# Kernel optimization log

Hardware: AMD Instinct MI355X
Metric: run time of the kernel (lower is better)

Reference implementation:

```python
import jax, jax.numpy as jnp
import numpy as np

B, L, E, H = 2, 2048, 1024, 16
HD = E // H  # 64
THETA = 10000.0


def setup_inputs() -> dict:
    key = jax.random.key(0)
    ks = jax.random.split(key, 9)
    s = 1.0 / np.sqrt(E)
    return {
        "x": jax.random.normal(ks[0], (B, L, E), jnp.float32),
        "Wq": jax.random.normal(ks[1], (E, E), jnp.float32) * s,
        "bq": jax.random.normal(ks[2], (E,), jnp.float32) * 0.01,
        "Wk": jax.random.normal(ks[3], (E, E), jnp.float32) * s,
        "bk": jax.random.normal(ks[4], (E,), jnp.float32) * 0.01,
        "Wv": jax.random.normal(ks[5], (E, E), jnp.float32) * s,
        "bv": jax.random.normal(ks[6], (E,), jnp.float32) * 0.01,
        "Wo": jax.random.normal(ks[7], (E, E), jnp.float32) * s,
        "bo": jax.random.normal(ks[8], (E,), jnp.float32) * 0.01,
    }


def _rope_tables(seq_len, dim, dtype):
    # lucidrains RotaryEmbedding: inv_freq over even indices, each freq repeated twice (interleaved)
    inv_freq = 1.0 / (THETA ** (jnp.arange(0, dim, 2, dtype=jnp.float32) / dim))
    freqs = jnp.arange(seq_len, dtype=jnp.float32)[:, None] * inv_freq[None, :]  # [L, dim/2]
    freqs = jnp.repeat(freqs, 2, axis=-1)  # [L, dim] -> f0,f0,f1,f1,...
    return jnp.cos(freqs).astype(dtype), jnp.sin(freqs).astype(dtype)


def _rotate_half(x):
    # interleaved pairs (x0, x1) -> (-x1, x0)
    x2 = x.reshape(*x.shape[:-1], -1, 2)
    x2 = jnp.stack([-x2[..., 1], x2[..., 0]], axis=-1)
    return x2.reshape(x.shape)


def _apply_rope(x, cos, sin):
    # x: [B, H, L, HD]; cos/sin: [L, HD]
    return x * cos[None, None] + _rotate_half(x) * sin[None, None]


def reference(x, Wq, bq, Wk, bk, Wv, bv, Wo, bo):
    b, l, e = x.shape
    q = (x @ Wq.T + bq).reshape(b, l, H, HD).transpose(0, 2, 1, 3)
    k = (x @ Wk.T + bk).reshape(b, l, H, HD).transpose(0, 2, 1, 3)
    v = (x @ Wv.T + bv).reshape(b, l, H, HD).transpose(0, 2, 1, 3)

    cos, sin = _rope_tables(l, HD, x.dtype)
    q = _apply_rope(q, cos, sin)
    k = _apply_rope(k, cos, sin)

    scale = 1.0 / np.sqrt(HD)
    scores = jnp.einsum("bhsd,bhed->bhse", q, k) * scale  # [B,H,L,L]
    attn = jax.nn.softmax(scores, axis=-1)
    out = jnp.einsum("bhse,bhed->bhsd", attn, v)  # [B,H,L,HD]
    out = out.transpose(0, 2, 1, 3).reshape(b, l, e)
    return out @ Wo.T + bo
```

## Files before the change

kernel.cpp:

```cpp
#include <hip/hip_runtime.h>

typedef unsigned short u16;
typedef __bf16 bf16x8 __attribute__((ext_vector_type(8)));
typedef float f32x4 __attribute__((ext_vector_type(4)));

#define LOG2E 1.4426950408889634f
#define EXP2(x) __builtin_amdgcn_exp2f(x)
#define NFM (-11.0f * LOG2E)

__device__ __forceinline__ u16 f2bf(float f) {
  unsigned int u = __float_as_uint(f);
  u += 0x7fffu + ((u >> 16) & 1u);
  return (u16)(u >> 16);
}

__device__ __forceinline__ void gld16(u16* lds, const u16* g) {
  __builtin_amdgcn_global_load_lds((const __attribute__((address_space(1))) unsigned int*)g,
                                   (__attribute__((address_space(3))) unsigned int*)lds,
                                   16, 0, 0);
}

__device__ __forceinline__ bf16x8 ldsv(const u16* p) {
  return *(const bf16x8*)p;
}

union U8 { uint4 u; bf16x8 v; };

__global__ __launch_bounds__(256) void k_prep(const float* __restrict__ x,
    const float* __restrict__ wq, const float* __restrict__ wk,
    const float* __restrict__ wv, const float* __restrict__ wo,
    u16* __restrict__ xb, u16* __restrict__ wqkvb, u16* __restrict__ wob) {
  unsigned gid = blockIdx.x * 256u + threadIdx.x;
  const float4* src;
  u16* dst;
  unsigned off;
  if (gid < 1048576u)      { src = (const float4*)x;  dst = xb;              off = gid; }
  else if (gid < 1310720u) { src = (const float4*)wq; dst = wqkvb;           off = gid - 1048576u; }
  else if (gid < 1572864u) { src = (const float4*)wk; dst = wqkvb + 1048576; off = gid - 1310720u; }
  else if (gid < 1835008u) { src = (const float4*)wv; dst = wqkvb + 2097152; off = gid - 1572864u; }
  else                     { src = (const float4*)wo; dst = wob;             off = gid - 1835008u; }
  float4 f = src[off];
  ushort4 o;
  o.x = f2bf(f.x); o.y = f2bf(f.y); o.z = f2bf(f.z); o.w = f2bf(f.w);
  ((ushort4*)dst)[off] = o;
}

__global__ __launch_bounds__(256) void k_rope(float* __restrict__ cosT, float* __restrict__ sinT) {
  int t = blockIdx.x * 256 + threadIdx.x;
  int l = t >> 5, i = t & 31;
  float inv = powf(10000.0f, -(float)i * (1.0f / 32.0f));
  float ang = (float)l * inv;
  float s, c;
  sincosf(ang, &s, &c);
  cosT[t] = c;
  sinT[t] = s;
}

__device__ __forceinline__ void gemm_loop(const u16* __restrict__ A, const u16* __restrict__ B,
                                          int m0, int n0, u16* As, u16* Bs, f32x4 acc[4][4]) {
  const int tid = threadIdx.x;
  const int lane = tid & 63, wave = tid >> 6;
  const int quad = lane >> 4, l16 = lane & 15;
  const int wm = wave & 1, wn = wave >> 1;

#pragma unroll
  for (int i = 0; i < 4; ++i)
#pragma unroll
    for (int j = 0; j < 4; ++j)
      acc[i][j] = (f32x4){0.f, 0.f, 0.f, 0.f};

  for (int kt = 0; kt < 16; ++kt) {
    int kb = kt * 64;
#pragma unroll
    for (int it = 0; it < 4; ++it) {
      int idx = it * 256 + tid;
      int row = idx >> 3, c8 = idx & 7;
      gld16(As + idx * 8, A + (long)(m0 + row) * 1024 + kb + c8 * 8);
      gld16(Bs + idx * 8, B + (long)(n0 + row) * 1024 + kb + c8 * 8);
    }
    __syncthreads();
#pragma unroll
    for (int kk = 0; kk < 2; ++kk) {
      bf16x8 a[4], b[4];
#pragma unroll
      for (int i = 0; i < 4; ++i)
        a[i] = ldsv(As + (wm * 64 + i * 16 + l16) * 64 + kk * 32 + quad * 8);
#pragma unroll
      for (int j = 0; j < 4; ++j)
        b[j] = ldsv(Bs + (wn * 64 + j * 16 + l16) * 64 + kk * 32 + quad * 8);
#pragma unroll
      for (int i = 0; i < 4; ++i)
#pragma unroll
        for (int j = 0; j < 4; ++j)
          acc[i][j] = __builtin_amdgcn_mfma_f32_16x16x32_bf16(a[i], b[j], acc[i][j], 0, 0, 0);
    }
    __syncthreads();
  }
}

__global__ __launch_bounds__(256) void k_qkv(const u16* __restrict__ xb, const u16* __restrict__ wqkvb,
    const float* __restrict__ bq, const float* __restrict__ bk, const float* __restrict__ bv,
    const float* __restrict__ cosT, const float* __restrict__ sinT,
    u16* __restrict__ Qg, u16* __restrict__ Kg, u16* __restrict__ VTg) {
  __shared__ __align__(16) u16 S[128 * 132];
  u16* As = S;
  u16* Bs = S + 8192;
  f32x4 acc[4][4];
  int m0 = blockIdx.y * 128, n0 = blockIdx.x * 128;
  gemm_loop(xb, wqkvb, m0, n0, As, Bs, acc);

  const int tid = threadIdx.x, lane = tid & 63, wave = tid >> 6;
  const int quad = lane >> 4, l16 = lane & 15;
  const int wm = wave & 1, wn = wave >> 1;
  const int qsel = n0 >> 10;
  const int b = m0 >> 11;
  const int mb0 = m0 & 2047;

  if (qsel < 2) {
    const float* bp = qsel ? bk : bq;
#pragma unroll
    for (int j = 0; j < 4; ++j) {
      int nl = wn * 64 + j * 16 + l16;
      int n = n0 + nl;
      int fcol = n & 1023;
      int d = fcol & 63;
      int pi = d >> 1;
      float bias = bp[fcol];
      float sgn = (d & 1) ? 1.0f : -1.0f;
#pragma unroll
      for (int i = 0; i < 4; ++i) {
#pragma unroll
        for (int r = 0; r < 4; ++r) {
          int ml = wm * 64 + i * 16 + quad * 4 + r;
          int l = mb0 + ml;
          float v = acc[i][j][r] + bias;
          float partner = __shfl_xor(v, 1);
          float c = cosT[l * 32 + pi], s = sinT[l * 32 + pi];
          float o = fmaf(v, c, sgn * partner * s);
          if (qsel == 0) o *= 0.125f;
          S[ml * 132 + nl] = f2bf(o);
        }
      }
    }
    __syncthreads();
    u16* dstb = (qsel == 0) ? Qg : Kg;
#pragma unroll
    for (int t = 0; t < 16; ++t) {
      int idx = t * 256 + tid;
      int ml = idx >> 5, c4 = idx & 31;
      int n = n0 + c4 * 4;
      int h = (n & 1023) >> 6;
      int d = n & 63;
      *(uint2*)(dstb + (((long)b * 16 + h) * 2048 + mb0 + ml) * 64 + d) =
          *(const uint2*)(S + ml * 132 + c4 * 4);
    }
  } else {
#pragma unroll
    for (int j = 0; j < 4; ++j) {
      int nl = wn * 64 + j * 16 + l16;
      float bias = bv[(n0 + nl) & 1023];
#pragma unroll
      for (int i = 0; i < 4; ++i) {
        int mb = wm * 64 + i * 16 + quad * 4;
        unsigned u0 = (unsigned)f2bf(acc[i][j][0] + bias) | ((unsigned)f2bf(acc[i][j][1] + bias) << 16);
        unsigned u1 = (unsigned)f2bf(acc[i][j][2] + bias) | ((unsigned)f2bf(acc[i][j][3] + bias) << 16);
        *(uint2*)(S + nl * 132 + mb) = make_uint2(u0, u1);
      }
    }
    __syncthreads();
#pragma unroll
    for (int t = 0; t < 16; ++t) {
      int idx = t * 256 + tid;
      int nl = idx >> 5, c4 = idx & 31;
      int vcol = (n0 & 1023) + nl;
      int h = vcol >> 6, d = vcol & 63;
      *(uint2*)(VTg + (((long)b * 16 + h) * 64 + d) * 2048 + mb0 + c4 * 4) =
          *(const uint2*)(S + nl * 132 + c4 * 4);
    }
  }
}

__global__ __launch_bounds__(256, 2) void k_attn(const u16* __restrict__ Qg, const u16* __restrict__ Kg,
    const u16* __restrict__ VTg, u16* __restrict__ Ctx) {
  __shared__ __align__(16) char smem[34816];
  u16* Ks = (u16*)smem;
  u16* Vs = (u16*)(smem + 16384);
  const int tid = threadIdx.x, lane = tid & 63, wave = tid >> 6;
  const int quad = lane >> 4, l16 = lane & 15;
  const int wm = wave & 1, wsn = wave >> 1;
  const int bh = blockIdx.y;
  const int m0 = blockIdx.x * 128;
  const u16* Qb = Qg + (long)bh * 2048 * 64;
  const u16* Kb = Kg + (long)bh * 2048 * 64;
  const u16* Vb = VTg + (long)bh * 64 * 2048;

  bf16x8 qf[4][2];
#pragma unroll
  for (int mt = 0; mt < 4; ++mt)
#pragma unroll
    for (int kk = 0; kk < 2; ++kk)
      qf[mt][kk] = *(const bf16x8*)(Qb + (long)(m0 + wm * 64 + mt * 16 + l16) * 64 + kk * 32 + quad * 8);

  f32x4 oacc[4][4];
  float rs[4];
#pragma unroll
  for (int dt = 0; dt < 4; ++dt)
#pragma unroll
    for (int mt = 0; mt < 4; ++mt)
      oacc[dt][mt] = (f32x4){0.f, 0.f, 0.f, 0.f};
#pragma unroll
  for (int mt = 0; mt < 4; ++mt) rs[mt] = 0.f;

  for (int st = 0; st < 16; ++st) {
    int s0 = st * 128;
#pragma unroll
    for (int it = 0; it < 4; ++it) {
      int idx = it * 256 + tid;
      int row = idx >> 3, c8 = idx & 7;
      gld16(Ks + idx * 8, Kb + (long)(s0 + row) * 64 + c8 * 8);
    }
#pragma unroll
    for (int it = 0; it < 4; ++it) {
      int idx = it * 256 + tid;
      int row = idx >> 4, g = idx & 15;
      uint4 vv = *(const uint4*)(Vb + (long)row * 2048 + s0 + g * 8);
      u16* wp = Vs + row * 132 + g * 8;
      *(uint2*)wp = make_uint2(vv.x, vv.y);
      *(uint2*)(wp + 4) = make_uint2(vv.z, vv.w);
    }
    __syncthreads();

    f32x4 sacc[4][4];
#pragma unroll
    for (int ct = 0; ct < 4; ++ct)
#pragma unroll
      for (int mt = 0; mt < 4; ++mt)
        sacc[ct][mt] = (f32x4){0.f, 0.f, 0.f, 0.f};
#pragma unroll
    for (int kk = 0; kk < 2; ++kk) {
      bf16x8 kf[4];
#pragma unroll
      for (int ct = 0; ct < 4; ++ct)
        kf[ct] = ldsv(Ks + (wsn * 64 + ct * 16 + l16) * 64 + kk * 32 + quad * 8);
#pragma unroll
      for (int ct = 0; ct < 4; ++ct)
#pragma unroll
        for (int mt = 0; mt < 4; ++mt)
          sacc[ct][mt] = __builtin_amdgcn_mfma_f32_16x16x32_bf16(kf[ct], qf[mt][kk], sacc[ct][mt], 0, 0, 0);
    }

#pragma unroll
    for (int c = 0; c < 2; ++c) {
      unsigned pk[2][4][2];
#pragma unroll
      for (int t = 0; t < 2; ++t) {
        int ct = c * 2 + t;
#pragma unroll
        for (int mt = 0; mt < 4; ++mt) {
          unsigned b[4];
          float sum = 0.f;
#pragma unroll
          for (int r = 0; r < 4; ++r) {
            float e = EXP2(fmaf(sacc[ct][mt][r], LOG2E, NFM));
            b[r] = __float_as_uint(e);
            sum += __uint_as_float(b[r] & 0xffff0000u);
          }
          rs[mt] += sum;
          pk[t][mt][0] = __builtin_amdgcn_perm(b[1], b[0], 0x07060302u);
          pk[t][mt][1] = __builtin_amdgcn_perm(b[3], b[2], 0x07060302u);
        }
      }
#pragma unroll
      for (int dt = 0; dt < 4; ++dt) {
        const u16* vp = Vs + (dt * 16 + l16) * 132 + wsn * 64 + c * 32 + quad * 4;
        uint2 lo = *(const uint2*)vp;
        uint2 hi = *(const uint2*)(vp + 16);
        U8 vfu; vfu.u = make_uint4(lo.x, lo.y, hi.x, hi.y);
#pragma unroll
        for (int mt = 0; mt < 4; ++mt) {
          U8 pfu; pfu.u = make_uint4(pk[0][mt][0], pk[0][mt][1], pk[1][mt][0], pk[1][mt][1]);
          oacc[dt][mt] = __builtin_amdgcn_mfma_f32_16x16x32_bf16(vfu.v, pfu.v, oacc[dt][mt], 0, 0, 0);
        }
      }
    }
    __syncthreads();
  }

  float* mbuf = (float*)smem;
  if (wsn == 1) {
#pragma unroll
    for (int dt = 0; dt < 4; ++dt)
#pragma unroll
      for (int mt = 0; mt < 4; ++mt)
#pragma unroll
        for (int r = 0; r < 4; ++r)
          mbuf[(wm * 68 + dt * 16 + mt * 4 + r) * 64 + lane] = oacc[dt][mt][r];
#pragma unroll
    for (int mt = 0; mt < 4; ++mt)
      mbuf[(wm * 68 + 64 + mt) * 64 + lane] = rs[mt];
  }
  __syncthreads();
  if (wsn == 0) {
#pragma unroll
    for (int dt = 0; dt < 4; ++dt)
#pragma unroll
      for (int mt = 0; mt < 4; ++mt)
#pragma unroll
        for (int r = 0; r < 4; ++r)
          oacc[dt][mt][r] += mbuf[(wm * 68 + dt * 16 + mt * 4 + r) * 64 + lane];
#pragma unroll
    for (int mt = 0; mt < 4; ++mt) {
      rs[mt] += mbuf[(wm * 68 + 64 + mt) * 64 + lane];
      rs[mt] += __shfl_xor(rs[mt], 16);
      rs[mt] += __shfl_xor(rs[mt], 32);
    }
    const int b = bh >> 4, h = bh & 15;
#pragma unroll
    for (int mt = 0; mt < 4; ++mt) {
      float inv = 1.0f / rs[mt];
      int tok = m0 + wm * 64 + mt * 16 + l16;
      u16* cp = Ctx + ((long)(b * 2048 + tok)) * 1024 + h * 64 + quad * 4;
#pragma unroll
      for (int dt = 0; dt < 4; ++dt) {
        float o0 = oacc[dt][mt][0] * inv, o1 = oacc[dt][mt][1] * inv;
        float o2 = oacc[dt][mt][2] * inv, o3 = oacc[dt][mt][3] * inv;
        unsigned u0 = (unsigned)f2bf(o0) | ((unsigned)f2bf(o1) << 16);
        unsigned u1 = (unsigned)f2bf(o2) | ((unsigned)f2bf(o3) << 16);
        *(uint2*)(cp + dt * 16) = make_uint2(u0, u1);
      }
    }
  }
}

__global__ __launch_bounds__(256) void k_out(const u16* __restrict__ Ctx, const u16* __restrict__ wob,
    const float* __restrict__ bo, float* __restrict__ out) {
  __shared__ __align__(16) u16 As[128 * 64];
  __shared__ __align__(16) u16 Bs[128 * 64];
  f32x4 acc[4][4];
  int m0 = blockIdx.y * 128, n0 = blockIdx.x * 128;
  gemm_loop(Ctx, wob, m0, n0, As, Bs, acc);
  const int tid = threadIdx.x, lane = tid & 63, wave = tid >> 6;
  const int quad = lane >> 4, l16 = lane & 15;
  const int wm = wave & 1, wn = wave >> 1;
#pragma unroll
  for (int i = 0; i < 4; ++i)
#pragma unroll
    for (int j = 0; j < 4; ++j) {
      int n = n0 + wn * 64 + j * 16 + l16;
      float b_ = bo[n];
#pragma unroll
      for (int r = 0; r < 4; ++r) {
        int m = m0 + wm * 64 + i * 16 + quad * 4 + r;
        out[(long)m * 1024 + n] = acc[i][j][r] + b_;
      }
    }
}

extern "C" void kernel_launch(void* const* d_in, const int* in_sizes, int n_in,
                              void* d_out, int out_size, void* d_ws, size_t ws_size,
                              hipStream_t stream) {
  const float* x  = (const float*)d_in[0];
  const float* Wq = (const float*)d_in[1];
  const float* bq = (const float*)d_in[2];
  const float* Wk = (const float*)d_in[3];
  const float* bk = (const float*)d_in[4];
  const float* Wv = (const float*)d_in[5];
  const float* bv = (const float*)d_in[6];
  const float* Wo = (const float*)d_in[7];
  const float* bo = (const float*)d_in[8];
  float* out = (float*)d_out;

  char* ws = (char*)d_ws;
  u16* xb    = (u16*)(ws);
  u16* wqkvb = (u16*)(ws + (8ul << 20));
  u16* wob   = (u16*)(ws + (14ul << 20));
  u16* Qg    = (u16*)(ws + (16ul << 20));
  u16* Kg    = (u16*)(ws + (24ul << 20));
  u16* VTg   = (u16*)(ws + (32ul << 20));
  u16* Ctx   = (u16*)(ws + (40ul << 20));
  float* cosT = (float*)(ws + (48ul << 20));
  float* sinT = (float*)(ws + (48ul << 20) + (256ul << 10));

  k_prep<<<dim3(8192), dim3(256), 0, stream>>>(x, Wq, Wk, Wv, Wo, xb, wqkvb, wob);
  k_rope<<<dim3(256), dim3(256), 0, stream>>>(cosT, sinT);
  k_qkv<<<dim3(24, 32), dim3(256), 0, stream>>>(xb, wqkvb, bq, bk, bv, cosT, sinT, Qg, Kg, VTg);
  k_attn<<<dim3(16, 32), dim3(256), 0, stream>>>(Qg, Kg, VTg, Ctx);
  k_out<<<dim3(8, 32), dim3(256), 0, stream>>>(Ctx, wob, bo, out);
}
```

Measured before the change: 220.3 us.

## Fuse rope table into prep, halve attention/out-proj M tiles, swizzle K LDS

Folds the RoPE cos/sin table generation into the prep conversion kernel, removing one launch. Halves the attention query tile to 64 rows, doubles the grid, and raises launch bounds to 4 blocks per CU for more occupancy. It also XOR-swizzles the K tile in LDS to reduce bank conflicts. The output projection moves to 64-row tiles with an inlined GEMM loop so more blocks fill the GPU. The trade-off is less reuse of each K/V tile per block, so global and LDS traffic per output rises.

```diff
diff --git a/kernel.cpp b/kernel.cpp
--- a/kernel.cpp
+++ b/kernel.cpp
@@ -29,8 +29,20 @@
 __global__ __launch_bounds__(256) void k_prep(const float* __restrict__ x,
     const float* __restrict__ wq, const float* __restrict__ wk,
     const float* __restrict__ wv, const float* __restrict__ wo,
-    u16* __restrict__ xb, u16* __restrict__ wqkvb, u16* __restrict__ wob) {
+    u16* __restrict__ xb, u16* __restrict__ wqkvb, u16* __restrict__ wob,
+    float* __restrict__ cosT, float* __restrict__ sinT) {
   unsigned gid = blockIdx.x * 256u + threadIdx.x;
+  if (gid >= 2097152u) {
+    int t = gid - 2097152u;
+    int l = t >> 5, i = t & 31;
+    float inv = powf(10000.0f, -(float)i * (1.0f / 32.0f));
+    float ang = (float)l * inv;
+    float s, c;
+    sincosf(ang, &s, &c);
+    cosT[t] = c;
+    sinT[t] = s;
+    return;
+  }
   const float4* src;
   u16* dst;
   unsigned off;
@@ -45,17 +57,6 @@
   ((ushort4*)dst)[off] = o;
 }
 
-__global__ __launch_bounds__(256) void k_rope(float* __restrict__ cosT, float* __restrict__ sinT) {
-  int t = blockIdx.x * 256 + threadIdx.x;
-  int l = t >> 5, i = t & 31;
-  float inv = powf(10000.0f, -(float)i * (1.0f / 32.0f));
-  float ang = (float)l * inv;
-  float s, c;
-  sincosf(ang, &s, &c);
-  cosT[t] = c;
-  sinT[t] = s;
-}
-
 __device__ __forceinline__ void gemm_loop(const u16* __restrict__ A, const u16* __restrict__ B,
                                           int m0, int n0, u16* As, u16* Bs, f32x4 acc[4][4]) {
   const int tid = threadIdx.x;
@@ -180,7 +181,7 @@
   }
 }
 
-__global__ __launch_bounds__(256, 2) void k_attn(const u16* __restrict__ Qg, const u16* __restrict__ Kg,
+__global__ __launch_bounds__(256, 4) void k_attn(const u16* __restrict__ Qg, const u16* __restrict__ Kg,
     const u16* __restrict__ VTg, u16* __restrict__ Ctx) {
   __shared__ __align__(16) char smem[34816];
   u16* Ks = (u16*)smem;
@@ -188,28 +189,28 @@
   const int tid = threadIdx.x, lane = tid & 63, wave = tid >> 6;
   const int quad = lane >> 4, l16 = lane & 15;
   const int wm = wave & 1, wsn = wave >> 1;
+  const int sw = l16 & 7;
   const int bh = blockIdx.y;
-  const int m0 = blockIdx.x * 128;
+  const int m0 = blockIdx.x * 64;
   const u16* Qb = Qg + (long)bh * 2048 * 64;
   const u16* Kb = Kg + (long)bh * 2048 * 64;
   const u16* Vb = VTg + (long)bh * 64 * 2048;
 
-  bf16x8 qf[4][2];
-#pragma unroll
-  for (int mt = 0; mt < 4; ++mt)
+  bf16x8 qf[2][2];
+#pragma unroll
+  for (int mt = 0; mt < 2; ++mt)
 #pragma unroll
     for (int kk = 0; kk < 2; ++kk)
-      qf[mt][kk] = *(const bf16x8*)(Qb + (long)(m0 + wm * 64 + mt * 16 + l16) * 64 + kk * 32 + quad * 8);
-
-  f32x4 oacc[4][4];
-  float rs[4];
+      qf[mt][kk] = *(const bf16x8*)(Qb + (long)(m0 + wm * 32 + mt * 16 + l16) * 64 + kk * 32 + quad * 8);
+
+  f32x4 oacc[4][2];
+  float rs[2];
 #pragma unroll
   for (int dt = 0; dt < 4; ++dt)
 #pragma unroll
-    for (int mt = 0; mt < 4; ++mt)
+    for (int mt = 0; mt < 2; ++mt)
       oacc[dt][mt] = (f32x4){0.f, 0.f, 0.f, 0.f};
-#pragma unroll
-  for (int mt = 0; mt < 4; ++mt) rs[mt] = 0.f;
+  rs[0] = rs[1] = 0.f;
 
   for (int st = 0; st < 16; ++st) {
     int s0 = st * 128;
@@ -217,7 +218,8 @@
     for (int it = 0; it < 4; ++it) {
       int idx = it * 256 + tid;
       int row = idx >> 3, c8 = idx & 7;
-      gld16(Ks + idx * 8, Kb + (long)(s0 + row) * 64 + c8 * 8);
+      int sc = c8 ^ (row & 7);
+      gld16(Ks + idx * 8, Kb + (long)(s0 + row) * 64 + sc * 8);
     }
 #pragma unroll
     for (int it = 0; it < 4; ++it) {
@@ -230,33 +232,34 @@
     }
     __syncthreads();
 
-    f32x4 sacc[4][4];
+    f32x4 sacc[4][2];
 #pragma unroll
     for (int ct = 0; ct < 4; ++ct)
 #pragma unroll
-      for (int mt = 0; mt < 4; ++mt)
+      for (int mt = 0; mt < 2; ++mt)
         sacc[ct][mt] = (f32x4){0.f, 0.f, 0.f, 0.f};
 #pragma unroll
     for (int kk = 0; kk < 2; ++kk) {
+      int ch = (kk * 4 + quad) ^ sw;
       bf16x8 kf[4];
 #pragma unroll
       for (int ct = 0; ct < 4; ++ct)
-        kf[ct] = ldsv(Ks + (wsn * 64 + ct * 16 + l16) * 64 + kk * 32 + quad * 8);
+        kf[ct] = ldsv(Ks + (wsn * 64 + ct * 16 + l16) * 64 + ch * 8);
 #pragma unroll
       for (int ct = 0; ct < 4; ++ct)
 #pragma unroll
-        for (int mt = 0; mt < 4; ++mt)
+        for (int mt = 0; mt < 2; ++mt)
           sacc[ct][mt] = __builtin_amdgcn_mfma_f32_16x16x32_bf16(kf[ct], qf[mt][kk], sacc[ct][mt], 0, 0, 0);
     }
 
 #pragma unroll
     for (int c = 0; c < 2; ++c) {
-      unsigned pk[2][4][2];
+      unsigned pk[2][2][2];
 #pragma unroll
       for (int t = 0; t < 2; ++t) {
         int ct = c * 2 + t;
 #pragma unroll
-        for (int mt = 0; mt < 4; ++mt) {
+        for (int mt = 0; mt < 2; ++mt) {
           unsigned b[4];
           float sum = 0.f;
 #pragma unroll
@@ -277,7 +280,7 @@
         uint2 hi = *(const uint2*)(vp + 16);
         U8 vfu; vfu.u = make_uint4(lo.x, lo.y, hi.x, hi.y);
 #pragma unroll
-        for (int mt = 0; mt < 4; ++mt) {
+        for (int mt = 0; mt < 2; ++mt) {
           U8 pfu; pfu.u = make_uint4(pk[0][mt][0], pk[0][mt][1], pk[1][mt][0], pk[1][mt][1]);
           oacc[dt][mt] = __builtin_amdgcn_mfma_f32_16x16x32_bf16(vfu.v, pfu.v, oacc[dt][mt], 0, 0, 0);
         }
@@ -291,34 +294,34 @@
 #pragma unroll
     for (int dt = 0; dt < 4; ++dt)
 #pragma unroll
-      for (int mt = 0; mt < 4; ++mt)
+      for (int mt = 0; mt < 2; ++mt)
 #pragma unroll
         for (int r = 0; r < 4; ++r)
-          mbuf[(wm * 68 + dt * 16 + mt * 4 + r) * 64 + lane] = oacc[dt][mt][r];
-#pragma unroll
-    for (int mt = 0; mt < 4; ++mt)
-      mbuf[(wm * 68 + 64 + mt) * 64 + lane] = rs[mt];
+          mbuf[(wm * 34 + dt * 8 + mt * 4 + r) * 64 + lane] = oacc[dt][mt][r];
+#pragma unroll
+    for (int mt = 0; mt < 2; ++mt)
+      mbuf[(wm * 34 + 32 + mt) * 64 + lane] = rs[mt];
   }
   __syncthreads();
   if (wsn == 0) {
 #pragma unroll
     for (int dt = 0; dt < 4; ++dt)
 #pragma unroll
-      for (int mt = 0; mt < 4; ++mt)
+      for (int mt = 0; mt < 2; ++mt)
 #pragma unroll
         for (int r = 0; r < 4; ++r)
-          oacc[dt][mt][r] += mbuf[(wm * 68 + dt * 16 + mt * 4 + r) * 64 + lane];
-#pragma unroll
-    for (int mt = 0; mt < 4; ++mt) {
-      rs[mt] += mbuf[(wm * 68 + 64 + mt) * 64 + lane];
+          oacc[dt][mt][r] += mbuf[(wm * 34 + dt * 8 + mt * 4 + r) * 64 + lane];
+#pragma unroll
+    for (int mt = 0; mt < 2; ++mt) {
+      rs[mt] += mbuf[(wm * 34 + 32 + mt) * 64 + lane];
       rs[mt] += __shfl_xor(rs[mt], 16);
       rs[mt] += __shfl_xor(rs[mt], 32);
     }
     const int b = bh >> 4, h = bh & 15;
 #pragma unroll
-    for (int mt = 0; mt < 4; ++mt) {
+    for (int mt = 0; mt < 2; ++mt) {
       float inv = 1.0f / rs[mt];
-      int tok = m0 + wm * 64 + mt * 16 + l16;
+      int tok = m0 + wm * 32 + mt * 16 + l16;
       u16* cp = Ctx + ((long)(b * 2048 + tok)) * 1024 + h * 64 + quad * 4;
 #pragma unroll
       for (int dt = 0; dt < 4; ++dt) {
@@ -334,23 +337,63 @@
 
 __global__ __launch_bounds__(256) void k_out(const u16* __restrict__ Ctx, const u16* __restrict__ wob,
     const float* __restrict__ bo, float* __restrict__ out) {
-  __shared__ __align__(16) u16 As[128 * 64];
+  __shared__ __align__(16) u16 As[64 * 64];
   __shared__ __align__(16) u16 Bs[128 * 64];
-  f32x4 acc[4][4];
-  int m0 = blockIdx.y * 128, n0 = blockIdx.x * 128;
-  gemm_loop(Ctx, wob, m0, n0, As, Bs, acc);
-  const int tid = threadIdx.x, lane = tid & 63, wave = tid >> 6;
+  const int tid = threadIdx.x;
+  const int lane = tid & 63, wave = tid >> 6;
   const int quad = lane >> 4, l16 = lane & 15;
   const int wm = wave & 1, wn = wave >> 1;
-#pragma unroll
-  for (int i = 0; i < 4; ++i)
+  int m0 = blockIdx.y * 64, n0 = blockIdx.x * 128;
+
+  f32x4 acc[2][4];
+#pragma unroll
+  for (int i = 0; i < 2; ++i)
+#pragma unroll
+    for (int j = 0; j < 4; ++j)
+      acc[i][j] = (f32x4){0.f, 0.f, 0.f, 0.f};
+
+  for (int kt = 0; kt < 16; ++kt) {
+    int kb = kt * 64;
+#pragma unroll
+    for (int it = 0; it < 2; ++it) {
+      int idx = it * 256 + tid;
+      int row = idx >> 3, c8 = idx & 7;
+      gld16(As + idx * 8, Ctx + (long)(m0 + row) * 1024 + kb + c8 * 8);
+    }
+#pragma unroll
+    for (int it = 0; it < 4; ++it) {
+      int idx = it * 256 + tid;
+      int row = idx >> 3, c8 = idx & 7;
+      gld16(Bs + idx * 8, wob + (long)(n0 + row) * 1024 + kb + c8 * 8);
+    }
+    __syncthreads();
+#pragma unroll
+    for (int kk = 0; kk < 2; ++kk) {
+      bf16x8 a[2], b[4];
+#pragma unroll
+      for (int i = 0; i < 2; ++i)
+        a[i] = ldsv(As + (wm * 32 + i * 16 + l16) * 64 + kk * 32 + quad * 8);
+#pragma unroll
+      for (int j = 0; j < 4; ++j)
+        b[j] = ldsv(Bs + (wn * 64 + j * 16 + l16) * 64 + kk * 32 + quad * 8);
+#pragma unroll
+      for (int i = 0; i < 2; ++i)
+#pragma unroll
+        for (int j = 0; j < 4; ++j)
+          acc[i][j] = __builtin_amdgcn_mfma_f32_16x16x32_bf16(a[i], b[j], acc[i][j], 0, 0, 0);
+    }
+    __syncthreads();
+  }
+
+#pragma unroll
+  for (int i = 0; i < 2; ++i)
 #pragma unroll
     for (int j = 0; j < 4; ++j) {
       int n = n0 + wn * 64 + j * 16 + l16;
       float b_ = bo[n];
 #pragma unroll
       for (int r = 0; r < 4; ++r) {
-        int m = m0 + wm * 64 + i * 16 + quad * 4 + r;
+        int m = m0 + wm * 32 + i * 16 + quad * 4 + r;
         out[(long)m * 1024 + n] = acc[i][j][r] + b_;
       }
     }
@@ -381,9 +424,8 @@
   float* cosT = (float*)(ws + (48ul << 20));
   float* sinT = (float*)(ws + (48ul << 20) + (256ul << 10));
 
-  k_prep<<<dim3(8192), dim3(256), 0, stream>>>(x, Wq, Wk, Wv, Wo, xb, wqkvb, wob);
-  k_rope<<<dim3(256), dim3(256), 0, stream>>>(cosT, sinT);
+  k_prep<<<dim3(8448), dim3(256), 0, stream>>>(x, Wq, Wk, Wv, Wo, xb, wqkvb, wob, cosT, sinT);
   k_qkv<<<dim3(24, 32), dim3(256), 0, stream>>>(xb, wqkvb, bq, bk, bv, cosT, sinT, Qg, Kg, VTg);
-  k_attn<<<dim3(16, 32), dim3(256), 0, stream>>>(Qg, Kg, VTg, Ctx);
-  k_out<<<dim3(8, 32), dim3(256), 0, stream>>>(Ctx, wob, bo, out);
-}
+  k_attn<<<dim3(32, 32), dim3(256), 0, stream>>>(Qg, Kg, VTg, Ctx);
+  k_out<<<dim3(8, 64), dim3(256), 0, stream>>>(Ctx, wob, bo, out);
+}
```

Result: faster. 214.9 us (-2.5%).

## Swizzle K/V LDS layout, DMA V tiles, remap attention blocks, fuse rope into prep

Applied to the files above, without the earlier changes.

K and V tiles are now stored in LDS with an XOR-swizzled 16-byte chunk layout, so fragment reads avoid bank conflicts. V is loaded straight into LDS with global_load_lds instead of going through registers, which drops the padded 132 stride. Attention blocks are remapped so that blocks sharing a head are spread across the grid in a different order, likely for cache locality. The rope table kernel is folded into the prep kernel to remove one launch.

```diff
diff --git a/kernel.cpp b/kernel.cpp
--- a/kernel.cpp
+++ b/kernel.cpp
@@ -29,8 +29,20 @@
 __global__ __launch_bounds__(256) void k_prep(const float* __restrict__ x,
     const float* __restrict__ wq, const float* __restrict__ wk,
     const float* __restrict__ wv, const float* __restrict__ wo,
-    u16* __restrict__ xb, u16* __restrict__ wqkvb, u16* __restrict__ wob) {
+    u16* __restrict__ xb, u16* __restrict__ wqkvb, u16* __restrict__ wob,
+    float* __restrict__ cosT, float* __restrict__ sinT) {
   unsigned gid = blockIdx.x * 256u + threadIdx.x;
+  if (gid >= 2097152u) {
+    int t = gid - 2097152u;
+    int l = t >> 5, i = t & 31;
+    float inv = powf(10000.0f, -(float)i * (1.0f / 32.0f));
+    float ang = (float)l * inv;
+    float s, c;
+    sincosf(ang, &s, &c);
+    cosT[t] = c;
+    sinT[t] = s;
+    return;
+  }
   const float4* src;
   u16* dst;
   unsigned off;
@@ -45,17 +57,6 @@
   ((ushort4*)dst)[off] = o;
 }
 
-__global__ __launch_bounds__(256) void k_rope(float* __restrict__ cosT, float* __restrict__ sinT) {
-  int t = blockIdx.x * 256 + threadIdx.x;
-  int l = t >> 5, i = t & 31;
-  float inv = powf(10000.0f, -(float)i * (1.0f / 32.0f));
-  float ang = (float)l * inv;
-  float s, c;
-  sincosf(ang, &s, &c);
-  cosT[t] = c;
-  sinT[t] = s;
-}
-
 __device__ __forceinline__ void gemm_loop(const u16* __restrict__ A, const u16* __restrict__ B,
                                           int m0, int n0, u16* As, u16* Bs, f32x4 acc[4][4]) {
   const int tid = threadIdx.x;
@@ -188,8 +189,10 @@
   const int tid = threadIdx.x, lane = tid & 63, wave = tid >> 6;
   const int quad = lane >> 4, l16 = lane & 15;
   const int wm = wave & 1, wsn = wave >> 1;
-  const int bh = blockIdx.y;
-  const int m0 = blockIdx.x * 128;
+  const int sw = l16 & 7;
+  const int lin = blockIdx.y * 16 + blockIdx.x;
+  const int bh = (lin & 7) * 4 + ((lin >> 3) & 3);
+  const int m0 = (lin >> 5) * 128;
   const u16* Qb = Qg + (long)bh * 2048 * 64;
   const u16* Kb = Kg + (long)bh * 2048 * 64;
   const u16* Vb = VTg + (long)bh * 64 * 2048;
@@ -217,16 +220,15 @@
     for (int it = 0; it < 4; ++it) {
       int idx = it * 256 + tid;
       int row = idx >> 3, c8 = idx & 7;
-      gld16(Ks + idx * 8, Kb + (long)(s0 + row) * 64 + c8 * 8);
+      int sc = c8 ^ (row & 7);
+      gld16(Ks + idx * 8, Kb + (long)(s0 + row) * 64 + sc * 8);
     }
 #pragma unroll
     for (int it = 0; it < 4; ++it) {
       int idx = it * 256 + tid;
-      int row = idx >> 4, g = idx & 15;
-      uint4 vv = *(const uint4*)(Vb + (long)row * 2048 + s0 + g * 8);
-      u16* wp = Vs + row * 132 + g * 8;
-      *(uint2*)wp = make_uint2(vv.x, vv.y);
-      *(uint2*)(wp + 4) = make_uint2(vv.z, vv.w);
+      int d = idx >> 4, ch = idx & 15;
+      int sc = ch ^ (d & 7);
+      gld16(Vs + idx * 8, Vb + (long)d * 2048 + s0 + sc * 8);
     }
     __syncthreads();
 
@@ -238,10 +240,11 @@
         sacc[ct][mt] = (f32x4){0.f, 0.f, 0.f, 0.f};
 #pragma unroll
     for (int kk = 0; kk < 2; ++kk) {
+      int ch = (kk * 4 + quad) ^ sw;
       bf16x8 kf[4];
 #pragma unroll
       for (int ct = 0; ct < 4; ++ct)
-        kf[ct] = ldsv(Ks + (wsn * 64 + ct * 16 + l16) * 64 + kk * 32 + quad * 8);
+        kf[ct] = ldsv(Ks + (wsn * 64 + ct * 16 + l16) * 64 + ch * 8);
 #pragma unroll
       for (int ct = 0; ct < 4; ++ct)
 #pragma unroll
@@ -270,11 +273,13 @@
           pk[t][mt][1] = __builtin_amdgcn_perm(b[3], b[2], 0x07060302u);
         }
       }
+      int ch0 = wsn * 8 + c * 4 + (quad >> 1);
+      int off = (quad & 1) * 4;
 #pragma unroll
       for (int dt = 0; dt < 4; ++dt) {
-        const u16* vp = Vs + (dt * 16 + l16) * 132 + wsn * 64 + c * 32 + quad * 4;
-        uint2 lo = *(const uint2*)vp;
-        uint2 hi = *(const uint2*)(vp + 16);
+        const u16* vrow = Vs + (dt * 16 + l16) * 128;
+        uint2 lo = *(const uint2*)(vrow + ((ch0 ^ sw) * 8 + off));
+        uint2 hi = *(const uint2*)(vrow + (((ch0 + 2) ^ sw) * 8 + off));
         U8 vfu; vfu.u = make_uint4(lo.x, lo.y, hi.x, hi.y);
 #pragma unroll
         for (int mt = 0; mt < 4; ++mt) {
@@ -381,8 +386,7 @@
   float* cosT = (float*)(ws + (48ul << 20));
   float* sinT = (float*)(ws + (48ul << 20) + (256ul << 10));
 
-  k_prep<<<dim3(8192), dim3(256), 0, stream>>>(x, Wq, Wk, Wv, Wo, xb, wqkvb, wob);
-  k_rope<<<dim3(256), dim3(256), 0, stream>>>(cosT, sinT);
+  k_prep<<<dim3(8448), dim3(256), 0, stream>>>(x, Wq, Wk, Wv, Wo, xb, wqkvb, wob, cosT, sinT);
   k_qkv<<<dim3(24, 32), dim3(256), 0, stream>>>(xb, wqkvb, bq, bk, bv, cosT, sinT, Qg, Kg, VTg);
   k_attn<<<dim3(16, 32), dim3(256), 0, stream>>>(Qg, Kg, VTg, Ctx);
   k_out<<<dim3(8, 32), dim3(256), 0, stream>>>(Ctx, wob, bo, out);
```

Result: no change. 217.3 us (-1.4%).
